# Performance work log

Measured on AMD Instinct MI355X. Metric: run time of the kernel, lower is better.

## Reference

```python
import jax, jax.numpy as jnp
import numpy as np
from jax import lax

B, C_IN, H, W = 32, 128, 64, 64
E = 384           # embed_dim
EB = E // 3       # per-branch channels
RED = 16          # ChannelAttention reduction -> hidden 384//16 = 24


def _conv(x, w, b, k):
    # x: [B,C,H,W], w: [O,I,k,k] (OIHW), 'same' padding k//2, stride 1
    p = k // 2
    y = lax.conv_general_dilated(x, w, (1, 1), [(p, p), (p, p)],
                                 dimension_numbers=('NCHW', 'OIHW', 'NCHW'))
    return y + b[None, :, None, None]


def setup_inputs() -> dict:
    key = jax.random.key(0)
    ks = jax.random.split(key, 8)

    def he(k, shape, fan_k, cout):
        fan_out = fan_k * fan_k * cout
        return jax.random.normal(k, shape, jnp.float32) * np.sqrt(2.0 / fan_out)

    x = jax.random.normal(ks[0], (B, C_IN, H, W), jnp.float32)
    w3 = he(ks[1], (EB, C_IN, 3, 3), 3, EB)
    w5 = he(ks[2], (EB, C_IN, 5, 5), 5, EB)
    w7 = he(ks[3], (EB, C_IN, 7, 7), 7, EB)
    ca_w1 = jax.random.normal(ks[4], (E // RED, E), jnp.float32) * 0.02
    ca_w2 = jax.random.normal(ks[5], (E, E // RED), jnp.float32) * 0.02
    fusion_w = he(ks[6], (E, E), 1, E)
    return {
        'x': x,
        'w3': w3, 'b3': jnp.zeros((EB,), jnp.float32),
        'w5': w5, 'b5': jnp.zeros((EB,), jnp.float32),
        'w7': w7, 'b7': jnp.zeros((EB,), jnp.float32),
        'ca_w1': ca_w1, 'ca_w2': ca_w2,
        'fusion_w': fusion_w, 'fusion_b': jnp.zeros((E,), jnp.float32),
        'ln_g': jnp.ones((E,), jnp.float32), 'ln_b': jnp.zeros((E,), jnp.float32),
    }


def reference(x, w3, b3, w5, b5, w7, b7, ca_w1, ca_w2, fusion_w, fusion_b, ln_g, ln_b):
    # multi-scale conv branches (strides all 1 -> identical HxW, no interpolation needed)
    f3 = _conv(x, w3, b3, 3)
    f5 = _conv(x, w5, b5, 5)
    f7 = _conv(x, w7, b7, 7)
    fused = jnp.concatenate([f3, f5, f7], axis=1)        # [B, E, H, W]

    # ChannelAttention (CBAM-style): shared MLP over global avg & max pool, sigmoid gate
    avg = jnp.mean(fused, axis=(2, 3))                   # [B, E]
    mx = jnp.max(fused, axis=(2, 3))                     # [B, E]
    def mlp(v):
        return jax.nn.relu(v @ ca_w1.T) @ ca_w2.T
    attn = jax.nn.sigmoid(mlp(avg) + mlp(mx))            # [B, E]
    fused = fused * attn[:, :, None, None]

    # 1x1 fusion conv
    fused = jnp.einsum('bchw,oc->bohw', fused, fusion_w) + fusion_b[None, :, None, None]

    # flatten to tokens + LayerNorm
    Bb, Ee, Hh, Ww = fused.shape
    t = fused.reshape(Bb, Ee, Hh * Ww).transpose(0, 2, 1)  # [B, N, E]
    mu = jnp.mean(t, axis=-1, keepdims=True)
    var = jnp.var(t, axis=-1, keepdims=True)
    t = (t - mu) / jnp.sqrt(var + 1e-5) * ln_g + ln_b
    return t
```

## Files before the change

kernel.cpp:

```cpp
#include <hip/hip_runtime.h>

#define BB 32
#define CIN 128
#define HH 64
#define WW 64
#define EE 384
#define EBC 128
#define HID 24
#define NPIX (HH*WW)
#define NTOK (BB*NPIX)

typedef __attribute__((ext_vector_type(8))) short short8;
typedef __attribute__((ext_vector_type(4))) float f32x4;
typedef __attribute__((ext_vector_type(4))) unsigned short us4;

__device__ __forceinline__ unsigned short f2bf(float f) {
    unsigned u = __float_as_uint(f);
    unsigned r = u + 0x7fffu + ((u >> 16) & 1u);
    return (unsigned short)(r >> 16);
}
__device__ __forceinline__ float bf2f(unsigned short u) {
    return __uint_as_float(((unsigned)u) << 16);
}
__device__ __forceinline__ unsigned fmapu(float f) {
    unsigned u = __float_as_uint(f);
    return (u & 0x80000000u) ? ~u : (u | 0x80000000u);
}
__device__ __forceinline__ float funmap(unsigned u) {
    unsigned b = (u & 0x80000000u) ? (u ^ 0x80000000u) : ~u;
    return __uint_as_float(b);
}

__global__ void repack_x(const float* __restrict__ x, unsigned short* __restrict__ xh) {
    int y = blockIdx.x, b = blockIdx.y;
    __shared__ unsigned short t[CIN][WW + 6];
    const float* xp = x + (((size_t)b * CIN) * HH + y) * WW;
    #pragma unroll
    for (int it = 0; it < 32; ++it) {
        int xc = threadIdx.x & 63;
        int c = (threadIdx.x >> 6) + it * 4;
        t[c][xc] = f2bf(xp[(size_t)c * NPIX + xc]);
    }
    __syncthreads();
    unsigned short* op = xh + (((size_t)b * HH + y) * WW) * CIN;
    #pragma unroll
    for (int it = 0; it < 8; ++it) {
        int id = threadIdx.x + it * 256;
        int xc = id >> 5, c0 = (id & 31) * 4;
        us4 v = { t[c0][xc], t[c0 + 1][xc], t[c0 + 2][xc], t[c0 + 3][xc] };
        *(us4*)(op + xc * CIN + c0) = v;
    }
}

__global__ void repack_w(const float* __restrict__ w3, const float* __restrict__ w5,
                         const float* __restrict__ w7, const float* __restrict__ fw,
                         unsigned short* __restrict__ wrep, unsigned short* __restrict__ fwb,
                         float* __restrict__ psum, unsigned* __restrict__ pmax) {
    int idx = blockIdx.x * 256 + threadIdx.x;
    if (idx < 83 * 16384) {
        int j = idx & 7;
        int lane = (idx >> 3) & 63;
        int mt = (idx >> 9) & 7;
        int cb = (idx >> 12) & 3;
        int t = idx >> 14;
        int l16 = lane & 15, g4 = lane >> 4;
        int o = mt * 16 + l16;
        int c = cb * 32 + g4 * 8 + j;
        float v;
        if (t < 9)       { int tt = t;      int dy = tt / 3, dx = tt % 3; v = w3[((o * CIN + c) * 3 + dy) * 3 + dx]; }
        else if (t < 34) { int tt = t - 9;  int dy = tt / 5, dx = tt % 5; v = w5[((o * CIN + c) * 5 + dy) * 5 + dx]; }
        else             { int tt = t - 34; int dy = tt / 7, dx = tt % 7; v = w7[((o * CIN + c) * 7 + dy) * 7 + dx]; }
        wrep[idx] = f2bf(v);
    }
    if (idx < EE * EE) {
        int j = idx & 7;
        int lane = (idx >> 3) & 63;
        int mc = idx >> 9;
        int m = mc % 24, cb = mc / 24;
        int l16 = lane & 15, g4 = lane >> 4;
        int o = m * 16 + l16;
        int c = cb * 32 + g4 * 8 + j;
        fwb[idx] = f2bf(fw[o * EE + c]);
    }
    if (idx < BB * EE) { psum[idx] = 0.f; pmax[idx] = 0u; }
}

template <int KS>
__global__ __launch_bounds__(256, 2) void conv_mfma(
        const unsigned short* __restrict__ xh, const unsigned short* __restrict__ wrp,
        const float* __restrict__ bias, unsigned short* __restrict__ fused,
        float* __restrict__ psum, unsigned* __restrict__ pmax, int choff) {
    constexpr int PK = KS / 2;
    constexpr int RT = 4 + 2 * PK;
    constexpr int TPX = 64 + 2 * PK;
    constexpr int NCH = RT * 4 * TPX;
    constexpr int NT = KS * KS;

    __shared__ short8 smem[NCH];

    int b = blockIdx.z;
    int y0 = blockIdx.x * 4;
    int lane = threadIdx.x & 63, wv = threadIdx.x >> 6;
    int l16 = lane & 15, g4 = lane >> 4;

    f32x4 acc[8][4];
    #pragma unroll
    for (int i = 0; i < 8; ++i)
        #pragma unroll
        for (int j = 0; j < 4; ++j) acc[i][j] = (f32x4){0.f, 0.f, 0.f, 0.f};

    const unsigned short* xb = xh + (size_t)b * (HH * WW * CIN);
    const short8* wv8 = (const short8*)wrp;

    for (int cb = 0; cb < 4; ++cb) {
        if (cb) __syncthreads();
        for (int i = threadIdx.x; i < NCH; i += 256) {
            int g = i & 3;
            int rp = i >> 2;
            int p = rp % TPX;
            int r = rp / TPX;
            int iy = y0 + r - PK, ix = p - PK;
            short8 v = {};
            if ((unsigned)iy < (unsigned)HH && (unsigned)ix < (unsigned)WW)
                v = *(const short8*)(xb + ((iy * WW + ix) * CIN + cb * 32 + g * 8));
            smem[(r * 4 + g) * TPX + p] = v;
        }
        __syncthreads();

        short8 a0[8], a1[8];
        {
            const short8* wf = wv8 + ((size_t)(cb * 8)) * 64 + lane;
            #pragma unroll
            for (int mt = 0; mt < 8; ++mt) a0[mt] = wf[mt * 64];
        }
        #pragma unroll
        for (int t = 0; t < NT; ++t) {
            short8* ac = (t & 1) ? a1 : a0;
            short8* an = (t & 1) ? a0 : a1;
            if (t + 1 < NT) {
                const short8* wf = wv8 + ((size_t)(((t + 1) * 4 + cb) * 8)) * 64 + lane;
                #pragma unroll
                for (int mt = 0; mt < 8; ++mt) an[mt] = wf[mt * 64];
            }
            int dy = t / KS, dx = t % KS;
            int lrow = ((wv + dy) * 4 + g4) * TPX + l16 + dx;
            short8 bfv[4];
            #pragma unroll
            for (int nt = 0; nt < 4; ++nt) bfv[nt] = smem[lrow + nt * 16];
            #pragma unroll
            for (int nt = 0; nt < 4; ++nt)
                #pragma unroll
                for (int mt = 0; mt < 8; ++mt)
                    acc[mt][nt] = __builtin_amdgcn_mfma_f32_16x16x32_bf16(ac[mt], bfv[nt], acc[mt][nt], 0, 0, 0);
        }
    }

    int y = y0 + wv;
    #pragma unroll
    for (int mt = 0; mt < 8; ++mt) {
        int orow = mt * 16 + g4 * 4;
        f32x4 bv = *(const f32x4*)(bias + orow);
        float sacc[4] = {0.f, 0.f, 0.f, 0.f};
        float macc[4] = {-1e30f, -1e30f, -1e30f, -1e30f};
        #pragma unroll
        for (int nt = 0; nt < 4; ++nt) {
            int pix = y * WW + nt * 16 + l16;
            us4 pk;
            #pragma unroll
            for (int r = 0; r < 4; ++r) {
                float vv = acc[mt][nt][r] + bv[r];
                sacc[r] += vv;
                macc[r] = fmaxf(macc[r], vv);
                pk[r] = f2bf(vv);
            }
            *(us4*)(fused + ((size_t)(b * NPIX + pix)) * EE + choff + orow) = pk;
        }
        #pragma unroll
        for (int r = 0; r < 4; ++r) {
            float s = sacc[r], m = macc[r];
            #pragma unroll
            for (int sh = 1; sh < 16; sh <<= 1) {
                s += __shfl_xor(s, sh);
                m = fmaxf(m, __shfl_xor(m, sh));
            }
            if (l16 == 0) {
                atomicAdd(&psum[b * EE + choff + orow + r], s);
                atomicMax(&pmax[b * EE + choff + orow + r], fmapu(m));
            }
        }
    }
}

__global__ void attn_kernel(const float* __restrict__ psum, const unsigned* __restrict__ pmax,
                            const float* __restrict__ ca_w1, const float* __restrict__ ca_w2,
                            float* __restrict__ attn) {
    int b = blockIdx.x;
    __shared__ float av[EE], mxv[EE], hsum[HID];
    int t = threadIdx.x;
    if (t < EE) {
        av[t] = psum[b * EE + t] * (1.0f / (float)NPIX);
        mxv[t] = funmap(pmax[b * EE + t]);
    }
    __syncthreads();
    if (t < HID) {
        float sa = 0.f, sm = 0.f;
        for (int c = 0; c < EE; ++c) {
            float w = ca_w1[t * EE + c];
            sa += w * av[c];
            sm += w * mxv[c];
        }
        hsum[t] = fmaxf(sa, 0.f) + fmaxf(sm, 0.f);
    }
    __syncthreads();
    if (t < EE) {
        float s = 0.f;
        for (int h = 0; h < HID; ++h) s += ca_w2[t * HID + h] * hsum[h];
        attn[b * EE + t] = 1.f / (1.f + __expf(-s));
    }
}

#define BPITCH 392
__global__ __launch_bounds__(256, 2) void fuse_ln(
        const unsigned short* __restrict__ fused, const unsigned short* __restrict__ fwb,
        const float* __restrict__ attn,
        const float* __restrict__ fusion_b, const float* __restrict__ ln_g,
        const float* __restrict__ ln_b, float* __restrict__ out) {
    int b = blockIdx.y;
    int p0 = blockIdx.x * 64;
    int lane = threadIdx.x & 63, wv = threadIdx.x >> 6;
    int l16 = lane & 15, g4 = lane >> 4;

    __shared__ unsigned short sB[64 * BPITCH];
    __shared__ float sattn[EE];
    __shared__ float s_sum[4][64], s_sq[4][64], s_mean[64], s_rstd[64];

    for (int i = threadIdx.x; i < EE; i += 256) sattn[i] = attn[b * EE + i];
    __syncthreads();

    const unsigned short* fb = fused + ((size_t)(b * NPIX + p0)) * EE;
    for (int i = threadIdx.x; i < 64 * 48; i += 256) {
        int cg = i % 48, tok = i / 48;
        short8 raw = *(const short8*)(fb + tok * EE + cg * 8);
        short8 o;
        #pragma unroll
        for (int j = 0; j < 8; ++j)
            o[j] = (short)f2bf(bf2f((unsigned short)raw[j]) * sattn[cg * 8 + j]);
        *(short8*)(sB + tok * BPITCH + cg * 8) = o;
    }
    __syncthreads();

    f32x4 acc[6][4];
    #pragma unroll
    for (int i = 0; i < 6; ++i)
        #pragma unroll
        for (int j = 0; j < 4; ++j) acc[i][j] = (f32x4){0.f, 0.f, 0.f, 0.f};

    const short8* fw8 = (const short8*)fwb;
    for (int cb = 0; cb < 12; ++cb) {
        int c0 = cb * 32 + g4 * 8;
        short8 a[6];
        #pragma unroll
        for (int mt = 0; mt < 6; ++mt)
            a[mt] = fw8[(cb * 24 + wv * 6 + mt) * 64 + lane];
        #pragma unroll
        for (int nt = 0; nt < 4; ++nt) {
            short8 bf = *(const short8*)(sB + (nt * 16 + l16) * BPITCH + c0);
            #pragma unroll
            for (int mt = 0; mt < 6; ++mt)
                acc[mt][nt] = __builtin_amdgcn_mfma_f32_16x16x32_bf16(a[mt], bf, acc[mt][nt], 0, 0, 0);
        }
    }

    #pragma unroll
    for (int nt = 0; nt < 4; ++nt) {
        float ps = 0.f, pq = 0.f;
        #pragma unroll
        for (int mt = 0; mt < 6; ++mt) {
            int o = wv * 96 + mt * 16 + g4 * 4;
            f32x4 bv = *(const f32x4*)(fusion_b + o);
            #pragma unroll
            for (int r = 0; r < 4; ++r) {
                float v = acc[mt][nt][r] + bv[r];
                acc[mt][nt][r] = v;
                ps += v;
                pq += v * v;
            }
        }
        ps += __shfl_xor(ps, 16); pq += __shfl_xor(pq, 16);
        ps += __shfl_xor(ps, 32); pq += __shfl_xor(pq, 32);
        if (g4 == 0) { s_sum[wv][nt * 16 + l16] = ps; s_sq[wv][nt * 16 + l16] = pq; }
    }
    __syncthreads();
    if (threadIdx.x < 64) {
        int pix = threadIdx.x;
        float s = 0.f, q = 0.f;
        #pragma unroll
        for (int w = 0; w < 4; ++w) { s += s_sum[w][pix]; q += s_sq[w][pix]; }
        float mean = s * (1.0f / (float)EE);
        float var = q * (1.0f / (float)EE) - mean * mean;
        s_mean[pix] = mean;
        s_rstd[pix] = rsqrtf(var + 1e-5f);
    }
    __syncthreads();

    #pragma unroll
    for (int nt = 0; nt < 4; ++nt) {
        int pix = nt * 16 + l16;
        float mean = s_mean[pix], rstd = s_rstd[pix];
        size_t tokbase = ((size_t)(b * NPIX + p0 + pix)) * EE;
        #pragma unroll
        for (int mt = 0; mt < 6; ++mt) {
            int o = wv * 96 + mt * 16 + g4 * 4;
            f32x4 g = *(const f32x4*)(ln_g + o);
            f32x4 be = *(const f32x4*)(ln_b + o);
            f32x4 res;
            #pragma unroll
            for (int r = 0; r < 4; ++r)
                res[r] = (acc[mt][nt][r] - mean) * rstd * g[r] + be[r];
            *(f32x4*)(out + tokbase + o) = res;
        }
    }
}

extern "C" void kernel_launch(void* const* d_in, const int* in_sizes, int n_in,
                              void* d_out, int out_size, void* d_ws, size_t ws_size,
                              hipStream_t stream) {
    const float* x    = (const float*)d_in[0];
    const float* w3   = (const float*)d_in[1];
    const float* b3   = (const float*)d_in[2];
    const float* w5   = (const float*)d_in[3];
    const float* b5   = (const float*)d_in[4];
    const float* w7   = (const float*)d_in[5];
    const float* b7   = (const float*)d_in[6];
    const float* caw1 = (const float*)d_in[7];
    const float* caw2 = (const float*)d_in[8];
    const float* fw   = (const float*)d_in[9];
    const float* fbias= (const float*)d_in[10];
    const float* lng  = (const float*)d_in[11];
    const float* lnb  = (const float*)d_in[12];
    float* out = (float*)d_out;

    char* ws = (char*)d_ws;
    size_t off = 0;
    unsigned short* xh   = (unsigned short*)(ws + off); off += (size_t)BB * HH * WW * CIN * 2;
    unsigned short* wrep = (unsigned short*)(ws + off); off += (size_t)83 * EBC * CIN * 2;
    unsigned short* fwb  = (unsigned short*)(ws + off); off += (size_t)EE * EE * 2;
    unsigned short* fused= (unsigned short*)(ws + off); off += (size_t)NTOK * EE * 2;
    float*    psum = (float*)(ws + off);    off += (size_t)BB * EE * 4;
    unsigned* pmax = (unsigned*)(ws + off); off += (size_t)BB * EE * 4;
    float*    attn = (float*)(ws + off);    off += (size_t)BB * EE * 4;

    repack_x<<<dim3(HH, BB), 256, 0, stream>>>(x, xh);
    repack_w<<<dim3(5312), 256, 0, stream>>>(w3, w5, w7, fw, wrep, fwb, psum, pmax);

    conv_mfma<3><<<dim3(16, 1, BB), 256, 0, stream>>>(xh, wrep + 0 * 16384,  b3, fused, psum, pmax, 0);
    conv_mfma<5><<<dim3(16, 1, BB), 256, 0, stream>>>(xh, wrep + 9 * 16384,  b5, fused, psum, pmax, 128);
    conv_mfma<7><<<dim3(16, 1, BB), 256, 0, stream>>>(xh, wrep + 34 * 16384, b7, fused, psum, pmax, 256);

    attn_kernel<<<dim3(BB), 384, 0, stream>>>(psum, pmax, caw1, caw2, attn);
    fuse_ln<<<dim3(NPIX / 64, BB), 256, 0, stream>>>(fused, fwb, attn, fbias, lng, lnb, out);
}
```

Before: 712.7 us.

## Pre-pad input, use direct global-to-LDS loads, merge conv branches into one launch

The input repack now writes a zero-padded 72x70 bf16 layout, which removes the bounds checks from the conv tile loads. Tile staging now uses global_load_lds to copy straight into shared memory instead of going through registers. The three branch convolutions are merged into one launch whose grid interleaves branches, with the 7x7 branch first, so the load is balanced and more blocks are in flight. The LDS operand reads are moved ahead of the weight prefetch and separated from the MFMA block by a sched_barrier. The cost is a larger padded buffer and a fixed shared allocation sized for the 7x7 tile in every block.

```diff
diff --git a/kernel.cpp b/kernel.cpp
--- a/kernel.cpp
+++ b/kernel.cpp
@@ -10,6 +10,9 @@
 #define NPIX (HH*WW)
 #define NTOK (BB*NPIX)
 
+#define XW 70
+#define XH 72
+
 typedef __attribute__((ext_vector_type(8))) short short8;
 typedef __attribute__((ext_vector_type(4))) float f32x4;
 typedef __attribute__((ext_vector_type(4))) unsigned short us4;
@@ -32,7 +35,14 @@
 }
 
 __global__ void repack_x(const float* __restrict__ x, unsigned short* __restrict__ xh) {
-    int y = blockIdx.x, b = blockIdx.y;
+    int py = blockIdx.x, b = blockIdx.y;
+    int y = py - 3;
+    unsigned short* orow = xh + ((size_t)(b * XH + py)) * XW * CIN;
+    if ((unsigned)y >= (unsigned)HH) {
+        for (int i = threadIdx.x; i < XW * CIN / 8; i += 256)
+            ((short8*)orow)[i] = (short8){};
+        return;
+    }
     __shared__ unsigned short t[CIN][WW + 6];
     const float* xp = x + (((size_t)b * CIN) * HH + y) * WW;
     #pragma unroll
@@ -42,13 +52,18 @@
         t[c][xc] = f2bf(xp[(size_t)c * NPIX + xc]);
     }
     __syncthreads();
-    unsigned short* op = xh + (((size_t)b * HH + y) * WW) * CIN;
+    unsigned short* op = orow + 3 * CIN;
     #pragma unroll
     for (int it = 0; it < 8; ++it) {
         int id = threadIdx.x + it * 256;
         int xc = id >> 5, c0 = (id & 31) * 4;
         us4 v = { t[c0][xc], t[c0 + 1][xc], t[c0 + 2][xc], t[c0 + 3][xc] };
         *(us4*)(op + xc * CIN + c0) = v;
+    }
+    if (threadIdx.x < 96) {
+        int pxsel = threadIdx.x >> 4;
+        int px = pxsel < 3 ? pxsel : 64 + pxsel;
+        ((short8*)(orow + px * CIN))[threadIdx.x & 15] = (short8){};
     }
 }
 
@@ -85,21 +100,23 @@
     if (idx < BB * EE) { psum[idx] = 0.f; pmax[idx] = 0u; }
 }
 
+
+#define SMEM_CHUNKS 2832
+
 template <int KS>
-__global__ __launch_bounds__(256, 2) void conv_mfma(
-        const unsigned short* __restrict__ xh, const unsigned short* __restrict__ wrp,
+__device__ __forceinline__ void conv_branch(
+        const unsigned short* __restrict__ xb,
+        const short8* __restrict__ wv8,
         const float* __restrict__ bias, unsigned short* __restrict__ fused,
-        float* __restrict__ psum, unsigned* __restrict__ pmax, int choff) {
+        float* __restrict__ psum, unsigned* __restrict__ pmax,
+        int b, int y0, int choff, short8* smem) {
     constexpr int PK = KS / 2;
     constexpr int RT = 4 + 2 * PK;
     constexpr int TPX = 64 + 2 * PK;
     constexpr int NCH = RT * 4 * TPX;
     constexpr int NT = KS * KS;
-
-    __shared__ short8 smem[NCH];
-
-    int b = blockIdx.z;
-    int y0 = blockIdx.x * 4;
+    constexpr int NINSTR = (NCH + 63) / 64;
+
     int lane = threadIdx.x & 63, wv = threadIdx.x >> 6;
     int l16 = lane & 15, g4 = lane >> 4;
 
@@ -109,44 +126,44 @@
         #pragma unroll
         for (int j = 0; j < 4; ++j) acc[i][j] = (f32x4){0.f, 0.f, 0.f, 0.f};
 
-    const unsigned short* xb = xh + (size_t)b * (HH * WW * CIN);
-    const short8* wv8 = (const short8*)wrp;
-
     for (int cb = 0; cb < 4; ++cb) {
         if (cb) __syncthreads();
-        for (int i = threadIdx.x; i < NCH; i += 256) {
-            int g = i & 3;
-            int rp = i >> 2;
-            int p = rp % TPX;
-            int r = rp / TPX;
-            int iy = y0 + r - PK, ix = p - PK;
-            short8 v = {};
-            if ((unsigned)iy < (unsigned)HH && (unsigned)ix < (unsigned)WW)
-                v = *(const short8*)(xb + ((iy * WW + ix) * CIN + cb * 32 + g * 8));
-            smem[(r * 4 + g) * TPX + p] = v;
-        }
-        __syncthreads();
-
+        for (int k = wv; k < NINSTR; k += 4) {
+            int c = k * 64 + lane;
+            int rg = c / TPX;
+            int p = c - rg * TPX;
+            int r = rg >> 2;
+            int g = rg & 3;
+            const unsigned short* src = xb +
+                ((size_t)((y0 + r - PK + 3) * XW + (p - PK + 3))) * CIN + cb * 32 + g * 8;
+            short8* dst = smem + k * 64;
+            __builtin_amdgcn_global_load_lds(
+                (const __attribute__((address_space(1))) void*)src,
+                (__attribute__((address_space(3))) void*)dst, 16, 0, 0);
+        }
         short8 a0[8], a1[8];
         {
             const short8* wf = wv8 + ((size_t)(cb * 8)) * 64 + lane;
             #pragma unroll
             for (int mt = 0; mt < 8; ++mt) a0[mt] = wf[mt * 64];
         }
+        __syncthreads();
+
         #pragma unroll
         for (int t = 0; t < NT; ++t) {
             short8* ac = (t & 1) ? a1 : a0;
             short8* an = (t & 1) ? a0 : a1;
+            int dy = t / KS, dx = t % KS;
+            int lrow = ((wv + dy) * 4 + g4) * TPX + l16 + dx;
+            short8 bfv[4];
+            #pragma unroll
+            for (int nt = 0; nt < 4; ++nt) bfv[nt] = smem[lrow + nt * 16];
             if (t + 1 < NT) {
                 const short8* wf = wv8 + ((size_t)(((t + 1) * 4 + cb) * 8)) * 64 + lane;
                 #pragma unroll
                 for (int mt = 0; mt < 8; ++mt) an[mt] = wf[mt * 64];
             }
-            int dy = t / KS, dx = t % KS;
-            int lrow = ((wv + dy) * 4 + g4) * TPX + l16 + dx;
-            short8 bfv[4];
-            #pragma unroll
-            for (int nt = 0; nt < 4; ++nt) bfv[nt] = smem[lrow + nt * 16];
+            __builtin_amdgcn_sched_barrier(0);
             #pragma unroll
             for (int nt = 0; nt < 4; ++nt)
                 #pragma unroll
@@ -189,6 +206,24 @@
             }
         }
     }
+}
+
+__global__ __launch_bounds__(256, 2) void conv_all(
+        const unsigned short* __restrict__ xh, const unsigned short* __restrict__ wrep,
+        const float* __restrict__ b3, const float* __restrict__ b5, const float* __restrict__ b7,
+        unsigned short* __restrict__ fused, float* __restrict__ psum, unsigned* __restrict__ pmax) {
+    __shared__ short8 smem[SMEM_CHUNKS];
+    int z = blockIdx.z;
+    int br = z % 3;
+    int b = z / 3;
+    int y0 = blockIdx.x * 4;
+    const unsigned short* xb = xh + (size_t)b * (XH * XW * CIN);
+    if (br == 0)
+        conv_branch<7>(xb, (const short8*)(wrep + 34 * 16384), b7, fused, psum, pmax, b, y0, 256, smem);
+    else if (br == 1)
+        conv_branch<5>(xb, (const short8*)(wrep + 9 * 16384),  b5, fused, psum, pmax, b, y0, 128, smem);
+    else
+        conv_branch<3>(xb, (const short8*)(wrep + 0 * 16384),  b3, fused, psum, pmax, b, y0, 0, smem);
 }
 
 __global__ void attn_kernel(const float* __restrict__ psum, const unsigned* __restrict__ pmax,
@@ -342,7 +377,7 @@
 
     char* ws = (char*)d_ws;
     size_t off = 0;
-    unsigned short* xh   = (unsigned short*)(ws + off); off += (size_t)BB * HH * WW * CIN * 2;
+    unsigned short* xh   = (unsigned short*)(ws + off); off += (size_t)BB * XH * XW * CIN * 2;
     unsigned short* wrep = (unsigned short*)(ws + off); off += (size_t)83 * EBC * CIN * 2;
     unsigned short* fwb  = (unsigned short*)(ws + off); off += (size_t)EE * EE * 2;
     unsigned short* fused= (unsigned short*)(ws + off); off += (size_t)NTOK * EE * 2;
@@ -350,12 +385,10 @@
     unsigned* pmax = (unsigned*)(ws + off); off += (size_t)BB * EE * 4;
     float*    attn = (float*)(ws + off);    off += (size_t)BB * EE * 4;
 
-    repack_x<<<dim3(HH, BB), 256, 0, stream>>>(x, xh);
+    repack_x<<<dim3(XH, BB), 256, 0, stream>>>(x, xh);
     repack_w<<<dim3(5312), 256, 0, stream>>>(w3, w5, w7, fw, wrep, fwb, psum, pmax);
 
-    conv_mfma<3><<<dim3(16, 1, BB), 256, 0, stream>>>(xh, wrep + 0 * 16384,  b3, fused, psum, pmax, 0);
-    conv_mfma<5><<<dim3(16, 1, BB), 256, 0, stream>>>(xh, wrep + 9 * 16384,  b5, fused, psum, pmax, 128);
-    conv_mfma<7><<<dim3(16, 1, BB), 256, 0, stream>>>(xh, wrep + 34 * 16384, b7, fused, psum, pmax, 256);
+    conv_all<<<dim3(16, 1, 3 * BB), 256, 0, stream>>>(xh, wrep, b3, b5, b7, fused, psum, pmax);
 
     attn_kernel<<<dim3(BB), 384, 0, stream>>>(psum, pmax, caw1, caw2, attn);
     fuse_ln<<<dim3(NPIX / 64, BB), 256, 0, stream>>>(fused, fwb, attn, fbias, lng, lnb, out);
```

After: 689.2 us. 1.03x faster.
